# Performance work log

Measured on AMD Instinct MI355X. Metric: run time of the kernel, lower is better.

Reference implementation:

```python
import jax, jax.numpy as jnp
import numpy as np

GROUP_SIZE = 128

def setup_inputs() -> dict:
    key = jax.random.key(0)
    k1, k2, k3 = jax.random.split(key, 3)
    B, S, K, N = 4, 128, 4096, 11008
    num_groups = K // GROUP_SIZE
    x = jax.random.normal(k1, (B, S, K), dtype=jnp.float16)
    # packed int4 weights: each byte holds two nibbles (low = even k, high = odd k)
    weight_packed = jax.random.randint(k2, (N, K // 2), 0, 256, dtype=jnp.int32)
    scales = (jax.random.uniform(k3, (N, num_groups), dtype=jnp.float16) * jnp.float16(0.1))
    return {"x": x, "weight_packed": weight_packed, "scales": scales}

def reference(x, weight_packed, scales):
    # x: (B, S, K) fp16; weight_packed: (N, K//2) int in [0,256); scales: (N, K//group_size) fp16
    N, Kp = weight_packed.shape
    K = Kp * 2
    # Unpack nibbles: even k -> low nibble, odd k -> high nibble (interleaved along K)
    low = weight_packed & 0x0F
    high = (weight_packed >> 4) & 0x0F
    w_int = jnp.stack([low, high], axis=-1).reshape(N, K).astype(jnp.float32)  # (N, K)
    # Per-group dequantization: w = scale * (q - 8)
    scale_full = jnp.repeat(scales.astype(jnp.float32), GROUP_SIZE, axis=1)    # (N, K)
    w = scale_full * (w_int - 8.0)
    # fp32 accumulation, fp16 output (matches kernel: float accum, half store)
    y = jnp.einsum('bsk,nk->bsn', x.astype(jnp.float32), w)
    return y.astype(jnp.float16)
```

## Files before the change

### kernel.cpp

```cpp
#include <hip/hip_runtime.h>


typedef __attribute__((ext_vector_type(8)))  short short8;
typedef __attribute__((ext_vector_type(16))) float f32x16;
typedef __attribute__((ext_vector_type(4)))  float f32x4;
typedef __attribute__((ext_vector_type(4)))  int   i32x4;
typedef __attribute__((ext_vector_type(2)))  int   i32x2;

#define M_DIM 512
#define N_DIM 11008
#define K_DIM 4096
#define BM 128
#define BN 64
#define BK 64
#define PAD 8
#define THREADS 256
#define NTILE_M (M_DIM / BM)
#define NTILE_N (N_DIM / BN)
#define NTILES  (NTILE_M * NTILE_N)
#define KITERS  (K_DIM / BK)

#if defined(__has_builtin)
#  if __has_builtin(__builtin_amdgcn_cvt_pk_bf16_f32)
#    define HAVE_PK_BF16 1
#  endif
#endif
#ifndef HAVE_PK_BF16
#  define HAVE_PK_BF16 0
#endif

__device__ __forceinline__ unsigned int fbits(float f) {
    union { float f; unsigned int u; } c; c.f = f; return c.u;
}
__device__ __forceinline__ int pack2bf(float lo, float hi) {
#if HAVE_PK_BF16
    typedef __attribute__((ext_vector_type(2))) __bf16 bf16x2;
    bf16x2 p = __builtin_amdgcn_cvt_pk_bf16_f32(lo, hi);
    int r; __builtin_memcpy(&r, &p, 4);
    return r;
#else
    unsigned int ul = fbits(lo), uh = fbits(hi);
    unsigned int l = (ul + 0x7FFFu + ((ul >> 16) & 1u)) >> 16;
    unsigned int h = (uh + 0x7FFFu + ((uh >> 16) & 1u)) & 0xFFFF0000u;
    return (int)(h | l);
#endif
}

__global__ __launch_bounds__(THREADS)
void cvt_x(const float* __restrict__ x, unsigned short* __restrict__ xw)
{
    int idx = (blockIdx.x * THREADS + threadIdx.x) * 4;
    f32x4 v = *(const f32x4*)(x + idx);
    i32x2 p;
    p[0] = pack2bf(v[0], v[1]);
    p[1] = pack2bf(v[2], v[3]);
    *(i32x2*)(xw + idx) = p;
}

template<bool PRECVT>
__global__ __launch_bounds__(THREADS, 2)
void dq_gemm(const unsigned short* __restrict__ xw,
             const float* __restrict__ xf,
             const int* __restrict__ wp,
             const float* __restrict__ scales,
             float* __restrict__ out)
{
    __shared__ __align__(16) unsigned short sA[2][BM][BK + PAD];
    __shared__ __align__(16) unsigned short sB[2][BN][BK + PAD];

    const int t  = threadIdx.x;
    const int bx = blockIdx.x;

    const int xcd = bx & 7;
    const int w   = bx >> 3;
    const int g_  = (w >> 1) * 8 + xcd;
    const int nb  = g_ >> 1;
    const int m_idx = ((g_ & 1) << 1) | (w & 1);

    const int m0 = m_idx * BM;
    const int n0 = nb * BN;

    const int wave = t >> 6;
    const int lane = t & 63;
    const int wm = (wave & 1) * 64;
    const int wn = (wave >> 1) * 32;
    const int lr = lane & 31;
    const int lk = (lane >> 5) * 8;

    const int tr3 = t >> 3;
    const int tc8 = (t & 7) * 8;
    const int tc4 = (t & 7) * 4;

    i32x4 pa[4];
    f32x4 paf[8];
    i32x4 pb[2];
    float sc[2];

    auto LOAD = [&](int kk) {
        const int kb = kk * BK;
        if constexpr (PRECVT) {
            #pragma unroll
            for (int i = 0; i < 4; ++i)
                pa[i] = *(const i32x4*)(xw + (size_t)(m0 + i * 32 + tr3) * K_DIM + kb + tc8);
        } else {
            #pragma unroll
            for (int i = 0; i < 8; ++i) {
                int row = i * 16 + (t >> 4), col = (t & 15) * 4;
                paf[i] = *(const f32x4*)(xf + (size_t)(m0 + row) * K_DIM + kb + col);
            }
        }
        const int gq = kb >> 7;
        #pragma unroll
        for (int i = 0; i < 2; ++i) {
            pb[i] = *(const i32x4*)(wp + (size_t)(n0 + i * 32 + tr3) * (K_DIM / 2) + (kb >> 1) + tc4);
            sc[i] = scales[(size_t)(n0 + i * 32 + tr3) * (K_DIM / 128) + gq];
        }
    };

    auto WRITE = [&](int buf) {
        if constexpr (PRECVT) {
            #pragma unroll
            for (int i = 0; i < 4; ++i)
                *(i32x4*)&sA[buf][i * 32 + tr3][tc8] = pa[i];
        } else {
            #pragma unroll
            for (int i = 0; i < 8; ++i) {
                int row = i * 16 + (t >> 4), col = (t & 15) * 4;
                i32x2 p;
                p[0] = pack2bf(paf[i][0], paf[i][1]);
                p[1] = pack2bf(paf[i][2], paf[i][3]);
                *(i32x2*)&sA[buf][row][col] = p;
            }
        }
        #pragma unroll
        for (int i = 0; i < 2; ++i) {
            float s = sc[i], ns8 = s * -8.0f;
            i32x4 res;
            #pragma unroll
            for (int e = 0; e < 4; ++e) {
                int b = pb[i][e];
                res[e] = pack2bf((float)(b & 15) * s + ns8,
                                 (float)((b >> 4) & 15) * s + ns8);
            }
            *(i32x4*)&sB[buf][i * 32 + tr3][tc4 * 2] = res;
        }
    };

    f32x16 acc[2] = {};

    auto MFMA_PHASE = [&](int buf) {
        __builtin_amdgcn_s_setprio(1);
        #pragma unroll
        for (int ks = 0; ks < BK; ks += 16) {
            short8 a[2], b;
            #pragma unroll
            for (int i = 0; i < 2; ++i)
                a[i] = *(const short8*)&sA[buf][wm + i * 32 + lr][ks + lk];
            b = *(const short8*)&sB[buf][wn + lr][ks + lk];
            #pragma unroll
            for (int i = 0; i < 2; ++i)
                acc[i] = __builtin_amdgcn_mfma_f32_32x32x16_bf16(a[i], b, acc[i], 0, 0, 0);
        }
        __builtin_amdgcn_s_setprio(0);
    };

    LOAD(0);
    WRITE(0);
    __syncthreads();

    #pragma unroll 2
    for (int kk = 0; kk < KITERS - 1; ++kk) {
        const int cur = kk & 1;
        LOAD(kk + 1);
        MFMA_PHASE(cur);
        WRITE(cur ^ 1);
        __syncthreads();
    }
    MFMA_PHASE((KITERS - 1) & 1);

    const int rbase = (lane >> 5) * 4;
    #pragma unroll
    for (int i = 0; i < 2; ++i) {
        int mg0 = m0 + wm + i * 32 + rbase;
        int ng  = n0 + wn + lr;
        #pragma unroll
        for (int r = 0; r < 16; ++r)
            out[(size_t)(mg0 + (r & 3) + 8 * (r >> 2)) * N_DIM + ng] = acc[i][r];
    }
}

extern "C" void kernel_launch(void* const* d_in, const int* in_sizes, int n_in,
                              void* d_out, int out_size, void* d_ws, size_t ws_size,
                              hipStream_t stream) {
    (void)in_sizes; (void)n_in; (void)out_size;
    const float* x      = (const float*)d_in[0];
    const int*   wpck   = (const int*)d_in[1];
    const float* scales = (const float*)d_in[2];
    float*       out    = (float*)d_out;

    const size_t XW_BYTES = (size_t)M_DIM * K_DIM * 2;

    if (ws_size >= XW_BYTES) {
        unsigned short* xw = (unsigned short*)d_ws;
        cvt_x<<<(M_DIM * K_DIM) / (THREADS * 4), THREADS, 0, stream>>>(x, xw);
        dq_gemm<true><<<NTILES, THREADS, 0, stream>>>(xw, x, wpck, scales, out);
    } else {
        dq_gemm<false><<<NTILES, THREADS, 0, stream>>>(nullptr, x, wpck, scales, out);
    }
}
```

Measured before the change: 260.5 us.

## Pre-swizzle activations into MFMA fragment layout and load A directly from global

The conversion kernel now writes bf16 activations in a per-lane MFMA fragment order, so the GEMM reads its A operands straight from global or L2 with one 16-byte load per lane. This drops the A tile from shared memory, halving LDS use and the per-iteration A staging, and launch bounds raise the occupancy target to three blocks. The cost is that A loads are no longer prefetched a stage ahead, so MFMAs wait on global-memory latency inside the compute phase, and every wave re-reads A from cache instead of sharing it.

```diff
diff --git a/kernel.cpp b/kernel.cpp
--- a/kernel.cpp
+++ b/kernel.cpp
@@ -19,6 +19,7 @@
 #define NTILE_N (N_DIM / BN)
 #define NTILES  (NTILE_M * NTILE_N)
 #define KITERS  (K_DIM / BK)
+#define KB16    (K_DIM / 16)
 
 #if defined(__has_builtin)
 #  if __has_builtin(__builtin_amdgcn_cvt_pk_bf16_f32)
@@ -49,23 +50,32 @@
 __global__ __launch_bounds__(THREADS)
 void cvt_x(const float* __restrict__ x, unsigned short* __restrict__ xw)
 {
-    int idx = (blockIdx.x * THREADS + threadIdx.x) * 4;
-    f32x4 v = *(const f32x4*)(x + idx);
-    i32x2 p;
-    p[0] = pack2bf(v[0], v[1]);
-    p[1] = pack2bf(v[2], v[3]);
-    *(i32x2*)(xw + idx) = p;
+    int c    = blockIdx.x * THREADS + threadIdx.x;
+    int lane = c & 63;
+    int kb   = (c >> 6) & (KB16 - 1);
+    int mb   = c >> 14;
+    int m    = mb * 32 + (lane & 31);
+    int k    = kb * 16 + (lane >> 5) * 8;
+
+    const float* src = x + (size_t)m * K_DIM + k;
+    f32x4 v0 = *(const f32x4*)(src);
+    f32x4 v1 = *(const f32x4*)(src + 4);
+    i32x4 p;
+    p[0] = pack2bf(v0[0], v0[1]);
+    p[1] = pack2bf(v0[2], v0[3]);
+    p[2] = pack2bf(v1[0], v1[1]);
+    p[3] = pack2bf(v1[2], v1[3]);
+    *(i32x4*)(xw + (size_t)c * 8) = p;
 }
 
 template<bool PRECVT>
-__global__ __launch_bounds__(THREADS, 2)
+__global__ __launch_bounds__(THREADS, 3)
 void dq_gemm(const unsigned short* __restrict__ xw,
              const float* __restrict__ xf,
              const int* __restrict__ wp,
              const float* __restrict__ scales,
              float* __restrict__ out)
 {
-    __shared__ __align__(16) unsigned short sA[2][BM][BK + PAD];
     __shared__ __align__(16) unsigned short sB[2][BN][BK + PAD];
 
     const int t  = threadIdx.x;
@@ -88,27 +98,13 @@
     const int lk = (lane >> 5) * 8;
 
     const int tr3 = t >> 3;
-    const int tc8 = (t & 7) * 8;
     const int tc4 = (t & 7) * 4;
 
-    i32x4 pa[4];
-    f32x4 paf[8];
     i32x4 pb[2];
     float sc[2];
 
-    auto LOAD = [&](int kk) {
+    auto LOADB = [&](int kk) {
         const int kb = kk * BK;
-        if constexpr (PRECVT) {
-            #pragma unroll
-            for (int i = 0; i < 4; ++i)
-                pa[i] = *(const i32x4*)(xw + (size_t)(m0 + i * 32 + tr3) * K_DIM + kb + tc8);
-        } else {
-            #pragma unroll
-            for (int i = 0; i < 8; ++i) {
-                int row = i * 16 + (t >> 4), col = (t & 15) * 4;
-                paf[i] = *(const f32x4*)(xf + (size_t)(m0 + row) * K_DIM + kb + col);
-            }
-        }
         const int gq = kb >> 7;
         #pragma unroll
         for (int i = 0; i < 2; ++i) {
@@ -117,21 +113,7 @@
         }
     };
 
-    auto WRITE = [&](int buf) {
-        if constexpr (PRECVT) {
-            #pragma unroll
-            for (int i = 0; i < 4; ++i)
-                *(i32x4*)&sA[buf][i * 32 + tr3][tc8] = pa[i];
-        } else {
-            #pragma unroll
-            for (int i = 0; i < 8; ++i) {
-                int row = i * 16 + (t >> 4), col = (t & 15) * 4;
-                i32x2 p;
-                p[0] = pack2bf(paf[i][0], paf[i][1]);
-                p[1] = pack2bf(paf[i][2], paf[i][3]);
-                *(i32x2*)&sA[buf][row][col] = p;
-            }
-        }
+    auto WRITEB = [&](int buf) {
         #pragma unroll
         for (int i = 0; i < 2; ++i) {
             float s = sc[i], ns8 = s * -8.0f;
@@ -148,35 +130,51 @@
 
     f32x16 acc[2] = {};
 
-    auto MFMA_PHASE = [&](int buf) {
+    const short8* xa8 = (const short8*)xw;
+    const size_t abase = ((size_t)((m0 + wm) >> 5) * KB16) * 64 + lane;
+
+    auto MFMA_PHASE = [&](int buf, int kb) {
         __builtin_amdgcn_s_setprio(1);
         #pragma unroll
         for (int ks = 0; ks < BK; ks += 16) {
             short8 a[2], b;
-            #pragma unroll
-            for (int i = 0; i < 2; ++i)
-                a[i] = *(const short8*)&sA[buf][wm + i * 32 + lr][ks + lk];
+            if constexpr (PRECVT) {
+                const size_t ab = abase + (size_t)((kb + ks) >> 4) * 64;
+                a[0] = xa8[ab];
+                a[1] = xa8[ab + (size_t)KB16 * 64];
+            } else {
+                #pragma unroll
+                for (int i = 0; i < 2; ++i) {
+                    const float* src = xf + (size_t)(m0 + wm + i * 32 + lr) * K_DIM + kb + ks + lk;
+                    f32x4 v0 = *(const f32x4*)(src);
+                    f32x4 v1 = *(const f32x4*)(src + 4);
+                    i32x4 p;
+                    p[0] = pack2bf(v0[0], v0[1]);
+                    p[1] = pack2bf(v0[2], v0[3]);
+                    p[2] = pack2bf(v1[0], v1[1]);
+                    p[3] = pack2bf(v1[2], v1[3]);
+                    __builtin_memcpy(&a[i], &p, 16);
+                }
+            }
             b = *(const short8*)&sB[buf][wn + lr][ks + lk];
-            #pragma unroll
-            for (int i = 0; i < 2; ++i)
-                acc[i] = __builtin_amdgcn_mfma_f32_32x32x16_bf16(a[i], b, acc[i], 0, 0, 0);
+            acc[0] = __builtin_amdgcn_mfma_f32_32x32x16_bf16(a[0], b, acc[0], 0, 0, 0);
+            acc[1] = __builtin_amdgcn_mfma_f32_32x32x16_bf16(a[1], b, acc[1], 0, 0, 0);
         }
         __builtin_amdgcn_s_setprio(0);
     };
 
-    LOAD(0);
-    WRITE(0);
+    LOADB(0);
+    WRITEB(0);
     __syncthreads();
 
-    #pragma unroll 2
     for (int kk = 0; kk < KITERS - 1; ++kk) {
         const int cur = kk & 1;
-        LOAD(kk + 1);
-        MFMA_PHASE(cur);
-        WRITE(cur ^ 1);
+        LOADB(kk + 1);
+        MFMA_PHASE(cur, kk * BK);
+        WRITEB(cur ^ 1);
         __syncthreads();
     }
-    MFMA_PHASE((KITERS - 1) & 1);
+    MFMA_PHASE((KITERS - 1) & 1, (KITERS - 1) * BK);
 
     const int rbase = (lane >> 5) * 4;
     #pragma unroll
@@ -202,7 +200,7 @@
 
     if (ws_size >= XW_BYTES) {
         unsigned short* xw = (unsigned short*)d_ws;
-        cvt_x<<<(M_DIM * K_DIM) / (THREADS * 4), THREADS, 0, stream>>>(x, xw);
+        cvt_x<<<(M_DIM * K_DIM) / (THREADS * 8), THREADS, 0, stream>>>(x, xw);
         dq_gemm<true><<<NTILES, THREADS, 0, stream>>>(xw, x, wpck, scales, out);
     } else {
         dq_gemm<false><<<NTILES, THREADS, 0, stream>>>(nullptr, x, wpck, scales, out);
```

Result: faster. 254.6 us (-2.3%).
